# Performance work log

Measured on AMD Instinct MI355X. Metric: run time of the kernel, lower is better.

The kernel has to match this reference:

```python
import jax, jax.numpy as jnp
import numpy as np

CHUNK = 1024  # mirrors torch chunk_size; keeps per-step intermediate bounded


def _chunked_min_dist(source, target):
    # source: [N, d], target: [M, d] -> [N] min squared distance to target
    n, d = source.shape
    chunks = source.reshape(n // CHUNK, CHUNK, d)

    def step(chunk):
        # diff: [CHUNK, M, d]; dist: [CHUNK, M]
        diff = chunk[:, None, :] - target[None, :, :]
        dist = jnp.sum(diff * diff, axis=-1)
        return jnp.min(dist, axis=1)

    mins = jax.lax.map(step, chunks)  # [n//CHUNK, CHUNK]
    return mins.reshape(n)


def setup_inputs() -> dict:
    key = jax.random.key(0)
    k1, k2 = jax.random.split(key)
    pred = jax.random.normal(k1, (32768, 3), dtype=jnp.float32)
    target = jax.random.normal(k2, (32768, 3), dtype=jnp.float32)
    return {"pred": pred, "target": target}


def reference(pred, target):
    min_pred_to_target = _chunked_min_dist(pred, target)
    min_target_to_pred = _chunked_min_dist(target, pred)
    # reduction='mean'
    return min_pred_to_target.mean() + min_target_to_pred.mean()
```

## Files before the change

kernel.cpp:

```cpp
#include <hip/hip_runtime.h>

#define NPTS 32768
#define G 32
#define NCELL (G*G*G)
#define SSTR (NCELL + 1)
#define RANGE 4.5f
#define CELLW 0.28125f

typedef unsigned int u32;


__device__ __forceinline__ int cell_of(float v) {
    int c = (int)floorf((v + RANGE) * (G / (2.0f * RANGE)));
    return min(max(c, 0), G - 1);
}
__device__ __forceinline__ float cell_lo(int i) {
    return fmaf((float)i, CELLW, -RANGE);
}

__global__ __launch_bounds__(256)
void hist_k(const float* __restrict__ pred, const float* __restrict__ targ,
            u32* __restrict__ cnt, u32* __restrict__ strag_cnt,
            float* __restrict__ out) {
    int i = blockIdx.x * 256 + threadIdx.x;
    if (i == 0) { *out = 0.0f; *strag_cnt = 0u; }
    int cloud = i >> 15, k = i & (NPTS - 1);
    const float* p = cloud ? targ : pred;
    float x = p[3*k], y = p[3*k+1], z = p[3*k+2];
    int c = (cell_of(z) * G + cell_of(y)) * G + cell_of(x);
    atomicAdd(&cnt[cloud * NCELL + c], 1u);
}

__global__ __launch_bounds__(1024)
void scan_k(const u32* __restrict__ cnt, u32* __restrict__ S, u32* __restrict__ cursor) {
    int cloud = blockIdx.x;
    const u32* c = cnt + cloud * NCELL;
    u32* s   = S + cloud * SSTR;
    u32* cur = cursor + cloud * NCELL;
    __shared__ u32 wt[16];
    int t = threadIdx.x, lane = t & 63, wave = t >> 6;

    u32 loc[32], run = 0;
    #pragma unroll
    for (int k = 0; k < 32; ++k) { loc[k] = run; run += c[32 * t + k]; }
    u32 inc = run;
    #pragma unroll
    for (int off = 1; off < 64; off <<= 1) {
        u32 nv = __shfl_up(inc, off, 64);
        if (lane >= off) inc += nv;
    }
    if (lane == 63) wt[wave] = inc;
    __syncthreads();
    if (t == 0) {
        u32 a = 0;
        #pragma unroll
        for (int w = 0; w < 16; ++w) { u32 v = wt[w]; wt[w] = a; a += v; }
    }
    __syncthreads();
    u32 tb = wt[wave] + (inc - run);
    #pragma unroll
    for (int k = 0; k < 32; ++k) {
        u32 v = tb + loc[k];
        s[32 * t + k] = v; cur[32 * t + k] = v;
    }
    if (t == 1023) s[NCELL] = NPTS;
}

__global__ __launch_bounds__(256)
void scatter_k(const float* __restrict__ pred, const float* __restrict__ targ,
               u32* __restrict__ cursor,
               float4* __restrict__ sortedA, float4* __restrict__ sortedB) {
    int i = blockIdx.x * 256 + threadIdx.x;
    int cloud = i >> 15, k = i & (NPTS - 1);
    const float* p = cloud ? targ : pred;
    float x = p[3*k], y = p[3*k+1], z = p[3*k+2];
    int c = (cell_of(z) * G + cell_of(y)) * G + cell_of(x);
    u32 pos = atomicAdd(&cursor[cloud * NCELL + c], 1u);
    (cloud ? sortedB : sortedA)[pos] = make_float4(x, y, z, 0.0f);
}

__device__ __forceinline__ float box_bound(int cx, int cy, int cz, float4 q, int R) {
    float bd = 3.4e38f;
    if (cx - R > 0)     bd = fminf(bd, q.x - cell_lo(cx - R));
    if (cx + R < G - 1) bd = fminf(bd, cell_lo(cx + R + 1) - q.x);
    if (cy - R > 0)     bd = fminf(bd, q.y - cell_lo(cy - R));
    if (cy + R < G - 1) bd = fminf(bd, cell_lo(cy + R + 1) - q.y);
    if (cz - R > 0)     bd = fminf(bd, q.z - cell_lo(cz - R));
    if (cz + R < G - 1) bd = fminf(bd, cell_lo(cz + R + 1) - q.z);
    return bd;
}

__global__ __launch_bounds__(256, 8)
void query_dense(const float4* __restrict__ sortedA, const float4* __restrict__ sortedB,
                 const u32* __restrict__ Sall, u32* __restrict__ strag_cnt,
                 u32* __restrict__ strag_list, float* __restrict__ out) {
    int tid = blockIdx.x * 256 + threadIdx.x;
    int sub = tid & 7;
    int qi = tid >> 3;
    int cloud = qi >> 15, k = qi & (NPTS - 1);
    const float4* Q = cloud ? sortedB : sortedA;
    const float4* T = cloud ? sortedA : sortedB;
    const u32* s = Sall + (cloud ^ 1) * SSTR;

    float4 q = Q[k];
    int cx = cell_of(q.x), cy = cell_of(q.y), cz = cell_of(q.z);
    int x0 = max(cx - 1, 0), x1 = min(cx + 1, G - 1);
    float best = 3.4e38f;

    int cbc = (cz * G + cy) * G;
    u32 cbeg = s[cbc + x0], cend = s[cbc + x1 + 1];
    u32 rb[9], re[9];
    #pragma unroll
    for (int i = 0; i < 9; ++i) {
        int dy = (i % 3) - 1, dz = (i / 3) - 1;
        int Y = cy + dy, Z = cz + dz;
        rb[i] = 0; re[i] = 0;
        if (i != 4 && (unsigned)Y < G && (unsigned)Z < G) {
            int cb = (Z * G + Y) * G;
            rb[i] = s[cb + x0]; re[i] = s[cb + x1 + 1];
        }
    }

    auto d2f = [&](float4 t) {
        float dx = q.x - t.x, dy = q.y - t.y, dz = q.z - t.z;
        return fmaf(dx, dx, fmaf(dy, dy, dz * dz));
    };
    auto scan_seg = [&](u32 beg, u32 end) {
        if (beg >= end) return;
        u32 half = (end - beg + 1) >> 1;
        u32 mid = beg + half;
        for (u32 o = sub; o < half; o += 8) {
            u32 ea = beg + o;
            u32 eb = min(mid + o, (u32)(NPTS - 1));
            float4 ta = T[ea];
            float4 tb = T[eb];
            float da = d2f(ta);
            float db = (mid + o < end) ? d2f(tb) : 3.4e38f;
            best = fminf(best, fminf(da, db));
        }
    };
    auto group_min = [&]() {
        best = fminf(best, __shfl_xor(best, 1, 64));
        best = fminf(best, __shfl_xor(best, 2, 64));
        best = fminf(best, __shfl_xor(best, 4, 64));
    };

    scan_seg(cbeg, cend);
    group_min();

    #pragma unroll
    for (int i = 0; i < 9; ++i) {
        if (i == 4) continue;
        int dy = (i % 3) - 1, dz = (i / 3) - 1;
        int Y = cy + dy, Z = cz + dz;
        if ((unsigned)Y >= G || (unsigned)Z >= G) continue;
        float ey = dy > 0 ? cell_lo(Y) - q.y : q.y - cell_lo(Y + 1);
        float ez = dz > 0 ? cell_lo(Z) - q.z : q.z - cell_lo(Z + 1);
        if (dy == 0) ey = 0.0f;
        if (dz == 0) ez = 0.0f;
        float mind2 = fmaf(ey, ey, ez * ez);
        if (mind2 < best) scan_seg(rb[i], re[i]);
    }
    group_min();

    float bd = box_bound(cx, cy, cz, q, 1);
    if (best > bd * bd) {
        if (sub == 0) {
            u32 slot = atomicAdd(strag_cnt, 1u);
            strag_list[slot] = (u32)qi;
        }
        best = 0.0f;
    }

    float v = best * 0.125f;
    #pragma unroll
    for (int off = 1; off < 64; off <<= 1)
        v += __shfl_xor(v, off, 64);
    __shared__ float wsum[4];
    int lane = threadIdx.x & 63, wave = threadIdx.x >> 6;
    if (lane == 0) wsum[wave] = v;
    __syncthreads();
    if (threadIdx.x == 0)
        atomicAdd(out, (wsum[0] + wsum[1] + wsum[2] + wsum[3]) * (1.0f / NPTS));
}

__global__ __launch_bounds__(256, 8)
void query_strag(const float4* __restrict__ sortedA, const float4* __restrict__ sortedB,
                 const u32* __restrict__ Sall, const u32* __restrict__ strag_cnt,
                 const u32* __restrict__ strag_list, float* __restrict__ out) {
    u32 n = *strag_cnt;
    int lane = threadIdx.x & 63;
    u32 wid = (blockIdx.x * 256 + threadIdx.x) >> 6;
    u32 nw = (gridDim.x * 256) >> 6;

    for (u32 idx = wid; idx < n; idx += nw) {
        u32 qi = strag_list[idx];
        int cloud = qi >> 15, k = qi & (NPTS - 1);
        const float4* Q = cloud ? sortedB : sortedA;
        const float4* T = cloud ? sortedA : sortedB;
        const u32* s = Sall + (cloud ^ 1) * SSTR;

        float4 q = Q[k];
        int cx = cell_of(q.x), cy = cell_of(q.y), cz = cell_of(q.z);
        int xlo = max(cx - 4, 0), xhi = min(cx + 4, G - 1);
        float best = 3.4e38f;

        u32 rb0 = 0, re0 = 0, rb1 = 0, re1 = 0;
        {
            int Z = cz + lane / 9 - 4, Y = cy + lane % 9 - 4;
            if ((unsigned)Z < G && (unsigned)Y < G) {
                int cb = (Z * G + Y) * G;
                rb0 = s[cb + xlo]; re0 = s[cb + xhi + 1];
            }
        }
        if (lane < 17) {
            int ri = lane + 64;
            int Z = cz + ri / 9 - 4, Y = cy + ri % 9 - 4;
            if ((unsigned)Z < G && (unsigned)Y < G) {
                int cb = (Z * G + Y) * G;
                rb1 = s[cb + xlo]; re1 = s[cb + xhi + 1];
            }
        }
        for (u32 e = rb0; e < re0; ++e) {
            float4 t = T[e];
            float dx = q.x - t.x, dy = q.y - t.y, dz = q.z - t.z;
            best = fminf(best, fmaf(dx, dx, fmaf(dy, dy, dz * dz)));
        }
        for (u32 e = rb1; e < re1; ++e) {
            float4 t = T[e];
            float dx = q.x - t.x, dy = q.y - t.y, dz = q.z - t.z;
            best = fminf(best, fmaf(dx, dx, fmaf(dy, dy, dz * dz)));
        }
        #pragma unroll
        for (int off = 1; off < 64; off <<= 1)
            best = fminf(best, __shfl_xor(best, off, 64));

        float bd4 = box_bound(cx, cy, cz, q, 4);
        if (best > bd4 * bd4) {
            int xlo9 = max(cx - 9, 0), xhi9 = min(cx + 9, G - 1);
            for (int j = 0; j < 6; ++j) {
                int ri = lane + 64 * j;
                if (ri >= 361) break;
                int Z = cz + ri / 19 - 9, Y = cy + ri % 19 - 9;
                if ((unsigned)Z < G && (unsigned)Y < G) {
                    int cb = (Z * G + Y) * G;
                    u32 b = s[cb + xlo9], e2 = s[cb + xhi9 + 1];
                    for (u32 e = b; e < e2; ++e) {
                        float4 t = T[e];
                        float dx = q.x - t.x, dy = q.y - t.y, dz = q.z - t.z;
                        best = fminf(best, fmaf(dx, dx, fmaf(dy, dy, dz * dz)));
                    }
                }
            }
            #pragma unroll
            for (int off = 1; off < 64; off <<= 1)
                best = fminf(best, __shfl_xor(best, off, 64));

            float bd9 = box_bound(cx, cy, cz, q, 9);
            if (best > bd9 * bd9) {
                auto d2 = [&](float4 t) {
                    float dx = q.x - t.x, dy = q.y - t.y, dz = q.z - t.z;
                    return fmaf(dx, dx, fmaf(dy, dy, dz * dz));
                };
                float a0 = 3.4e38f, a1 = 3.4e38f, a2 = 3.4e38f, a3 = 3.4e38f;
                #pragma unroll 2
                for (int blk = 0; blk < NPTS / 512; ++blk) {
                    u32 base = (u32)lane + (u32)blk * 512u;
                    float4 t0 = T[base];       float4 t1 = T[base + 64];
                    float4 t2 = T[base + 128]; float4 t3 = T[base + 192];
                    float4 t4 = T[base + 256]; float4 t5 = T[base + 320];
                    float4 t6 = T[base + 384]; float4 t7 = T[base + 448];
                    a0 = fminf(a0, d2(t0)); a1 = fminf(a1, d2(t1));
                    a2 = fminf(a2, d2(t2)); a3 = fminf(a3, d2(t3));
                    a0 = fminf(a0, d2(t4)); a1 = fminf(a1, d2(t5));
                    a2 = fminf(a2, d2(t6)); a3 = fminf(a3, d2(t7));
                }
                float bb = fminf(fminf(a0, a1), fminf(a2, a3));
                #pragma unroll
                for (int off = 1; off < 64; off <<= 1)
                    bb = fminf(bb, __shfl_xor(bb, off, 64));
                best = fminf(best, bb);
            }
        }

        if (lane == 0) atomicAdd(out, best * (1.0f / NPTS));
    }
}

extern "C" void kernel_launch(void* const* d_in, const int* in_sizes, int n_in,
                              void* d_out, int out_size, void* d_ws, size_t ws_size,
                              hipStream_t stream) {
    const float* pred = (const float*)d_in[0];
    const float* targ = (const float*)d_in[1];
    float* out = (float*)d_out;
    char* ws = (char*)d_ws;
    float4* sortedA = (float4*)(ws);
    float4* sortedB = (float4*)(ws + (512 << 10));
    u32* S         = (u32*)(ws + (1024 << 10));
    u32* cnt       = (u32*)(ws + (1344 << 10));
    u32* cursor    = (u32*)(ws + (1600 << 10));
    u32* strag_cnt = (u32*)(ws + (1856 << 10));
    u32* strag_list = cnt;

    hipMemsetAsync(cnt, 0, 2 * NCELL * sizeof(u32), stream);
    hist_k     <<<256, 256, 0, stream>>>(pred, targ, cnt, strag_cnt, out);
    scan_k     <<<2, 1024, 0, stream>>>(cnt, S, cursor);
    scatter_k  <<<256, 256, 0, stream>>>(pred, targ, cursor, sortedA, sortedB);
    query_dense<<<2048, 256, 0, stream>>>(sortedA, sortedB, S, strag_cnt, strag_list, out);
    query_strag<<<512, 256, 0, stream>>>(sortedA, sortedB, S, strag_cnt, strag_list, out);
}
```

Before: 166.1 us.

## Split straggler query into radius-4 pass and separate compacted brute-force kernel

Straggler queries whose radius-4 search cannot prove the minimum are no longer handled inline. They are appended to a compacted brute_list and processed by a new query_brute kernel, which runs the radius-9 search and, if needed, the full scan. The aim is to cut the divergence and tail imbalance that came from a few waves doing long fallbacks inside query_strag. The cost is an extra kernel launch and atomic list appends, and the radius-9 stage reruns without the radius-4 best as a starting value.

Result: slower. 198.0 us (+19.2%).

```diff
diff --git a/kernel.cpp b/kernel.cpp
--- a/kernel.cpp
+++ b/kernel.cpp
@@ -21,9 +21,9 @@
 __global__ __launch_bounds__(256)
 void hist_k(const float* __restrict__ pred, const float* __restrict__ targ,
             u32* __restrict__ cnt, u32* __restrict__ strag_cnt,
-            float* __restrict__ out) {
+            u32* __restrict__ brute_cnt, float* __restrict__ out) {
     int i = blockIdx.x * 256 + threadIdx.x;
-    if (i == 0) { *out = 0.0f; *strag_cnt = 0u; }
+    if (i == 0) { *out = 0.0f; *strag_cnt = 0u; *brute_cnt = 0u; }
     int cloud = i >> 15, k = i & (NPTS - 1);
     const float* p = cloud ? targ : pred;
     float x = p[3*k], y = p[3*k+1], z = p[3*k+2];
@@ -187,7 +187,8 @@
 __global__ __launch_bounds__(256, 8)
 void query_strag(const float4* __restrict__ sortedA, const float4* __restrict__ sortedB,
                  const u32* __restrict__ Sall, const u32* __restrict__ strag_cnt,
-                 const u32* __restrict__ strag_list, float* __restrict__ out) {
+                 const u32* __restrict__ strag_list, u32* __restrict__ brute_cnt,
+                 u32* __restrict__ brute_list, float* __restrict__ out) {
     u32 n = *strag_cnt;
     int lane = threadIdx.x & 63;
     u32 wid = (blockIdx.x * 256 + threadIdx.x) >> 6;
@@ -237,50 +238,79 @@
 
         float bd4 = box_bound(cx, cy, cz, q, 4);
         if (best > bd4 * bd4) {
-            int xlo9 = max(cx - 9, 0), xhi9 = min(cx + 9, G - 1);
-            for (int j = 0; j < 6; ++j) {
-                int ri = lane + 64 * j;
-                if (ri >= 361) break;
-                int Z = cz + ri / 19 - 9, Y = cy + ri % 19 - 9;
-                if ((unsigned)Z < G && (unsigned)Y < G) {
-                    int cb = (Z * G + Y) * G;
-                    u32 b = s[cb + xlo9], e2 = s[cb + xhi9 + 1];
-                    for (u32 e = b; e < e2; ++e) {
-                        float4 t = T[e];
-                        float dx = q.x - t.x, dy = q.y - t.y, dz = q.z - t.z;
-                        best = fminf(best, fmaf(dx, dx, fmaf(dy, dy, dz * dz)));
-                    }
+            if (lane == 0) {
+                u32 slot = atomicAdd(brute_cnt, 1u);
+                brute_list[slot] = qi;
+            }
+        } else {
+            if (lane == 0) atomicAdd(out, best * (1.0f / NPTS));
+        }
+    }
+}
+
+__global__ __launch_bounds__(256, 8)
+void query_brute(const float4* __restrict__ sortedA, const float4* __restrict__ sortedB,
+                 const u32* __restrict__ Sall, const u32* __restrict__ brute_cnt,
+                 const u32* __restrict__ brute_list, float* __restrict__ out) {
+    u32 n = *brute_cnt;
+    int lane = threadIdx.x & 63;
+    u32 wid = (blockIdx.x * 256 + threadIdx.x) >> 6;
+    u32 nw = (gridDim.x * 256) >> 6;
+
+    for (u32 idx = wid; idx < n; idx += nw) {
+        u32 qi = brute_list[idx];
+        int cloud = qi >> 15, k = qi & (NPTS - 1);
+        const float4* Q = cloud ? sortedB : sortedA;
+        const float4* T = cloud ? sortedA : sortedB;
+        const u32* s = Sall + (cloud ^ 1) * SSTR;
+
+        float4 q = Q[k];
+        int cx = cell_of(q.x), cy = cell_of(q.y), cz = cell_of(q.z);
+        float best = 3.4e38f;
+
+        int xlo9 = max(cx - 9, 0), xhi9 = min(cx + 9, G - 1);
+        for (int j = 0; j < 6; ++j) {
+            int ri = lane + 64 * j;
+            if (ri >= 361) break;
+            int Z = cz + ri / 19 - 9, Y = cy + ri % 19 - 9;
+            if ((unsigned)Z < G && (unsigned)Y < G) {
+                int cb = (Z * G + Y) * G;
+                u32 b = s[cb + xlo9], e2 = s[cb + xhi9 + 1];
+                for (u32 e = b; e < e2; ++e) {
+                    float4 t = T[e];
+                    float dx = q.x - t.x, dy = q.y - t.y, dz = q.z - t.z;
+                    best = fminf(best, fmaf(dx, dx, fmaf(dy, dy, dz * dz)));
                 }
             }
+        }
+        #pragma unroll
+        for (int off = 1; off < 64; off <<= 1)
+            best = fminf(best, __shfl_xor(best, off, 64));
+
+        float bd9 = box_bound(cx, cy, cz, q, 9);
+        if (best > bd9 * bd9) {
+            auto d2 = [&](float4 t) {
+                float dx = q.x - t.x, dy = q.y - t.y, dz = q.z - t.z;
+                return fmaf(dx, dx, fmaf(dy, dy, dz * dz));
+            };
+            float a0 = 3.4e38f, a1 = 3.4e38f, a2 = 3.4e38f, a3 = 3.4e38f;
+            #pragma unroll 2
+            for (int blk = 0; blk < NPTS / 512; ++blk) {
+                u32 base = (u32)lane + (u32)blk * 512u;
+                float4 t0 = T[base];       float4 t1 = T[base + 64];
+                float4 t2 = T[base + 128]; float4 t3 = T[base + 192];
+                float4 t4 = T[base + 256]; float4 t5 = T[base + 320];
+                float4 t6 = T[base + 384]; float4 t7 = T[base + 448];
+                a0 = fminf(a0, d2(t0)); a1 = fminf(a1, d2(t1));
+                a2 = fminf(a2, d2(t2)); a3 = fminf(a3, d2(t3));
+                a0 = fminf(a0, d2(t4)); a1 = fminf(a1, d2(t5));
+                a2 = fminf(a2, d2(t6)); a3 = fminf(a3, d2(t7));
+            }
+            float bb = fminf(fminf(a0, a1), fminf(a2, a3));
             #pragma unroll
             for (int off = 1; off < 64; off <<= 1)
-                best = fminf(best, __shfl_xor(best, off, 64));
-
-            float bd9 = box_bound(cx, cy, cz, q, 9);
-            if (best > bd9 * bd9) {
-                auto d2 = [&](float4 t) {
-                    float dx = q.x - t.x, dy = q.y - t.y, dz = q.z - t.z;
-                    return fmaf(dx, dx, fmaf(dy, dy, dz * dz));
-                };
-                float a0 = 3.4e38f, a1 = 3.4e38f, a2 = 3.4e38f, a3 = 3.4e38f;
-                #pragma unroll 2
-                for (int blk = 0; blk < NPTS / 512; ++blk) {
-                    u32 base = (u32)lane + (u32)blk * 512u;
-                    float4 t0 = T[base];       float4 t1 = T[base + 64];
-                    float4 t2 = T[base + 128]; float4 t3 = T[base + 192];
-                    float4 t4 = T[base + 256]; float4 t5 = T[base + 320];
-                    float4 t6 = T[base + 384]; float4 t7 = T[base + 448];
-                    a0 = fminf(a0, d2(t0)); a1 = fminf(a1, d2(t1));
-                    a2 = fminf(a2, d2(t2)); a3 = fminf(a3, d2(t3));
-                    a0 = fminf(a0, d2(t4)); a1 = fminf(a1, d2(t5));
-                    a2 = fminf(a2, d2(t6)); a3 = fminf(a3, d2(t7));
-                }
-                float bb = fminf(fminf(a0, a1), fminf(a2, a3));
-                #pragma unroll
-                for (int off = 1; off < 64; off <<= 1)
-                    bb = fminf(bb, __shfl_xor(bb, off, 64));
-                best = fminf(best, bb);
-            }
+                bb = fminf(bb, __shfl_xor(bb, off, 64));
+            best = fminf(best, bb);
         }
 
         if (lane == 0) atomicAdd(out, best * (1.0f / NPTS));
@@ -296,16 +326,20 @@
     char* ws = (char*)d_ws;
     float4* sortedA = (float4*)(ws);
     float4* sortedB = (float4*)(ws + (512 << 10));
-    u32* S         = (u32*)(ws + (1024 << 10));
-    u32* cnt       = (u32*)(ws + (1344 << 10));
-    u32* cursor    = (u32*)(ws + (1600 << 10));
-    u32* strag_cnt = (u32*)(ws + (1856 << 10));
+    u32* S          = (u32*)(ws + (1024 << 10));
+    u32* cnt        = (u32*)(ws + (1344 << 10));
+    u32* cursor     = (u32*)(ws + (1600 << 10));
+    u32* strag_cnt  = (u32*)(ws + (1856 << 10));
+    u32* brute_cnt  = strag_cnt + 1;
     u32* strag_list = cnt;
+    u32* brute_list = cursor;
 
     hipMemsetAsync(cnt, 0, 2 * NCELL * sizeof(u32), stream);
-    hist_k     <<<256, 256, 0, stream>>>(pred, targ, cnt, strag_cnt, out);
+    hist_k     <<<256, 256, 0, stream>>>(pred, targ, cnt, strag_cnt, brute_cnt, out);
     scan_k     <<<2, 1024, 0, stream>>>(cnt, S, cursor);
     scatter_k  <<<256, 256, 0, stream>>>(pred, targ, cursor, sortedA, sortedB);
     query_dense<<<2048, 256, 0, stream>>>(sortedA, sortedB, S, strag_cnt, strag_list, out);
-    query_strag<<<512, 256, 0, stream>>>(sortedA, sortedB, S, strag_cnt, strag_list, out);
-}
+    query_strag<<<512, 256, 0, stream>>>(sortedA, sortedB, S, strag_cnt, strag_list,
+                                         brute_cnt, brute_list, out);
+    query_brute<<<64, 256, 0, stream>>>(sortedA, sortedB, S, brute_cnt, brute_list, out);
+}
```
